# Kernel optimization log

Measured on AMD Instinct MI355X. Metric: run time of the kernel, lower is better.

## Reference

```python
import jax, jax.numpy as jnp
import numpy as np

B, S, D = 2, 2048, 1024
E, N, HID = 8, 4, 4096

def setup_inputs() -> dict:
    key = jax.random.key(0)
    ks = jax.random.split(key, 6)
    x = jax.random.normal(ks[0], (B, S, D), dtype=jnp.float32)
    w_router = jax.random.normal(ks[1], (E, D), dtype=jnp.float32) * 0.02
    A_fc = jax.random.normal(ks[2], (E, N, N, N), dtype=jnp.float32) * 0.5
    S_fc = jax.random.normal(ks[3], (E, N, HID // N, D // N), dtype=jnp.float32) * (1.0 / np.sqrt(D))
    A_proj = jax.random.normal(ks[4], (E, N, N, N), dtype=jnp.float32) * 0.5
    S_proj = jax.random.normal(ks[5], (E, N, D // N, HID // N), dtype=jnp.float32) * (1.0 / np.sqrt(HID))
    return {"x": x, "w_router": w_router, "A_fc": A_fc, "S_fc": S_fc, "A_proj": A_proj, "S_proj": S_proj}

def _phm(Xn, A, S):
    # Xn: [T, n, s_in], S: [n, s_out, s_in], A: [n, n, n] -> [T, n, s_out]
    T_ = jnp.einsum('bkl,iol->bkio', Xn, S)
    return jnp.einsum('ijk,bkio->bjo', A, T_)

def reference(x, w_router, A_fc, S_fc, A_proj, S_proj):
    e_num, n = A_fc.shape[0], A_fc.shape[1]
    d = x.shape[-1]
    flat = x.reshape(-1, d)                      # [T, D]
    T = flat.shape[0]
    logits = flat @ w_router.T                   # [T, E]
    probs = jax.nn.softmax(logits, axis=-1)
    expert_idx = jnp.argmax(logits, axis=-1)     # [T]
    tpe = jnp.zeros((e_num,), flat.dtype).at[expert_idx].add(1.0)
    frac = tpe / T
    aux_loss = jnp.sum(frac * probs.mean(axis=0)) * e_num
    Xn = flat.reshape(T, n, d // n)
    out = jnp.zeros_like(flat)
    for e in range(e_num):                        # small fixed expert loop
        h = _phm(Xn, A_fc[e], S_fc[e]).reshape(T, -1)   # [T, HID]
        h = jnp.where(h >= 0, h, 0.5 * h)               # leaky_relu slope 0.5
        Hn = (h * h).reshape(T, n, -1)
        y = _phm(Hn, A_proj[e], S_proj[e]).reshape(T, d)
        out = out + jnp.where((expert_idx == e)[:, None], y, jnp.zeros((), flat.dtype))
    return out.reshape(x.shape), aux_loss
```

## Files before the change

### kernel.cpp

```cpp
#include <hip/hip_runtime.h>
#include <hip/hip_bf16.h>


#define T_TOK 4096
#define DIM   1024
#define NEXP  8
#define HIDD  4096
#define SLOTS 5120

static constexpr size_t OFF_WFC   = 0;
static constexpr size_t OFF_WPROJ = 67108864ull;
static constexpr size_t OFF_XB    = 134217728ull;
static constexpr size_t OFF_H     = 144703488ull;
static constexpr size_t OFF_BSUM  = 186646528ull;
static constexpr size_t OFF_EIDX  = OFF_BSUM + 1024*8*8;
static constexpr size_t OFF_TOK   = OFF_EIDX + (size_t)T_TOK*4;
static constexpr size_t OFF_CNT   = OFF_TOK + (size_t)SLOTS*4;

typedef __attribute__((ext_vector_type(8))) short short8;
typedef __attribute__((ext_vector_type(4))) float f32x4;

static __device__ __forceinline__ ushort f2bf(float f) {
    __hip_bfloat16 h = __float2bfloat16(f);
    return __builtin_bit_cast(ushort, h);
}

static __device__ __forceinline__ void gload_lds16(const ushort* g, ushort* l) {
    __builtin_amdgcn_global_load_lds((const __attribute__((address_space(1))) void*)g,
                                     (__attribute__((address_space(3))) void*)l,
                                     16, 0, 0);
}

__global__ __launch_bounds__(256) void router_k(const float* __restrict__ x,
                                                const float* __restrict__ wr,
                                                double* __restrict__ bsum,
                                                int* __restrict__ eidx,
                                                ushort* __restrict__ xb)
{
    __shared__ double shp[4][8];
    int tid = threadIdx.x, w = tid >> 6, lane = tid & 63;
    int t = blockIdx.x * 4 + w;
    const float4* xr = (const float4*)(x + (size_t)t * DIM);
    float4 xv[4];
#pragma unroll
    for (int q = 0; q < 4; q++) xv[q] = xr[q * 64 + lane];
    ushort4* xo = (ushort4*)(xb + (size_t)t * DIM);
#pragma unroll
    for (int q = 0; q < 4; q++) {
        float4 v = xv[q];
        ushort4 bq;
        bq.x = f2bf(v.x); bq.y = f2bf(v.y); bq.z = f2bf(v.z); bq.w = f2bf(v.w);
        xo[q * 64 + lane] = bq;
    }
    double lg[8];
#pragma unroll
    for (int e = 0; e < 8; e++) {
        const float4* wv = (const float4*)(wr + (size_t)e * DIM);
        double s = 0.0;
#pragma unroll
        for (int q = 0; q < 4; q++) {
            float4 a = xv[q], b = wv[q * 64 + lane];
            s += (double)a.x * b.x + (double)a.y * b.y + (double)a.z * b.z + (double)a.w * b.w;
        }
#pragma unroll
        for (int d = 1; d < 64; d <<= 1) s += __shfl_xor(s, d);
        lg[e] = s;
    }
    double m = lg[0];
#pragma unroll
    for (int e = 1; e < 8; e++) m = lg[e] > m ? lg[e] : m;
    double ex[8], sum = 0.0;
#pragma unroll
    for (int e = 0; e < 8; e++) { ex[e] = exp(lg[e] - m); sum += ex[e]; }
    if (lane < 8) shp[w][lane] = ex[lane] / sum;
    if (lane == 0) {
        int am = 0; double bv = lg[0];
#pragma unroll
        for (int e = 1; e < 8; e++) if (lg[e] > bv) { bv = lg[e]; am = e; }
        eidx[t] = am;
    }
    __syncthreads();
    if (tid < 8)
        bsum[(size_t)blockIdx.x * 8 + tid] =
            shp[0][tid] + shp[1][tid] + shp[2][tid] + shp[3][tid];
}

__global__ __launch_bounds__(256) void plan_k(const double* __restrict__ bsum,
                                              const int* __restrict__ eidx,
                                              int* __restrict__ counts,
                                              int* __restrict__ offsets,
                                              int* __restrict__ tok,
                                              float* __restrict__ auxout)
{
    __shared__ int hist[256][8];
    __shared__ double red[256][8];
    __shared__ int offs[8];
    int tid = threadIdx.x;
    for (int i = tid; i < SLOTS; i += 256) tok[i] = -1;
    int base = tid * 16;
    int le[16];
    int lc[8] = {0,0,0,0,0,0,0,0};
#pragma unroll
    for (int j = 0; j < 16; j++) { le[j] = eidx[base + j]; lc[le[j]]++; }
#pragma unroll
    for (int e = 0; e < 8; e++) hist[tid][e] = lc[e];
    __syncthreads();
    for (int s = 1; s < 256; s <<= 1) {
        int v[8];
        if (tid >= s) {
#pragma unroll
            for (int e = 0; e < 8; e++) v[e] = hist[tid - s][e];
        }
        __syncthreads();
        if (tid >= s) {
#pragma unroll
            for (int e = 0; e < 8; e++) hist[tid][e] += v[e];
        }
        __syncthreads();
    }
    int myBase[8];
#pragma unroll
    for (int e = 0; e < 8; e++) myBase[e] = hist[tid][e] - lc[e];
    if (tid == 0) {
        int off = 0;
#pragma unroll
        for (int e = 0; e < 8; e++) {
            int c = hist[255][e];
            counts[e] = c;
            offsets[e] = off; offs[e] = off;
            off += (c + 127) & ~127;
        }
    }
    __syncthreads();
    int cur[8];
#pragma unroll
    for (int e = 0; e < 8; e++) cur[e] = myBase[e];
#pragma unroll
    for (int j = 0; j < 16; j++) {
        int e = le[j];
        tok[offs[e] + cur[e]++] = base + j;
    }
    double ps[8] = {0, 0, 0, 0, 0, 0, 0, 0};
    for (int b = tid; b < 1024; b += 256) {
#pragma unroll
        for (int e = 0; e < 8; e++) ps[e] += bsum[(size_t)b * 8 + e];
    }
#pragma unroll
    for (int e = 0; e < 8; e++) red[tid][e] = ps[e];
    __syncthreads();
    for (int s = 128; s > 0; s >>= 1) {
        if (tid < s) {
#pragma unroll
            for (int e = 0; e < 8; e++) red[tid][e] += red[tid + s][e];
        }
        __syncthreads();
    }
    if (tid == 0) {
        double aux = 0.0;
#pragma unroll
        for (int e = 0; e < 8; e++)
            aux += ((double)hist[255][e] / T_TOK) * (red[0][e] / T_TOK);
        auxout[0] = (float)(aux * NEXP);
    }
}

__global__ __launch_bounds__(256) void wmat_k(const float* __restrict__ Afc,
                                              const float* __restrict__ Sfc,
                                              const float* __restrict__ Apj,
                                              const float* __restrict__ Spj,
                                              ushort* __restrict__ Wfc,
                                              ushort* __restrict__ Wpj)
{
    __shared__ float Ash[64];
    int b = blockIdx.x;
    int tid = threadIdx.x;
    if (b < 8192) {
        int e = b >> 10, o = b & 1023;
        if (tid < 64) Ash[tid] = Afc[e * 64 + tid];
        __syncthreads();
        float s0 = Sfc[((size_t)(e * 4 + 0) * 1024 + o) * 256 + tid];
        float s1 = Sfc[((size_t)(e * 4 + 1) * 1024 + o) * 256 + tid];
        float s2 = Sfc[((size_t)(e * 4 + 2) * 1024 + o) * 256 + tid];
        float s3 = Sfc[((size_t)(e * 4 + 3) * 1024 + o) * 256 + tid];
        size_t base = (size_t)e * 4194304ull;
#pragma unroll
        for (int j = 0; j < 4; j++)
#pragma unroll
            for (int k = 0; k < 4; k++) {
                float v = Ash[j * 4 + k] * s0 + Ash[16 + j * 4 + k] * s1 +
                          Ash[32 + j * 4 + k] * s2 + Ash[48 + j * 4 + k] * s3;
                Wfc[base + (size_t)(j * 1024 + o) * 1024 + k * 256 + tid] = f2bf(v);
            }
    } else {
        int b2 = b - 8192;
        int e = b2 >> 8, o = b2 & 255;
        if (tid < 64) Ash[tid] = Apj[e * 64 + tid];
        __syncthreads();
        float s[4][4];
#pragma unroll
        for (int i = 0; i < 4; i++)
#pragma unroll
            for (int q = 0; q < 4; q++)
                s[i][q] = Spj[((size_t)(e * 4 + i) * 256 + o) * 1024 + q * 256 + tid];
        size_t base = (size_t)e * 4194304ull;
#pragma unroll
        for (int j = 0; j < 4; j++)
#pragma unroll
            for (int k = 0; k < 4; k++) {
                float a0 = Ash[j * 4 + k], a1 = Ash[16 + j * 4 + k];
                float a2 = Ash[32 + j * 4 + k], a3 = Ash[48 + j * 4 + k];
#pragma unroll
                for (int q = 0; q < 4; q++) {
                    float v = a0 * s[0][q] + a1 * s[1][q] + a2 * s[2][q] + a3 * s[3][q];
                    Wpj[base + (size_t)(j * 256 + o) * 4096 + k * 1024 + q * 256 + tid] = f2bf(v);
                }
            }
    }
}

template <int KDIM, int NDIM, int BM, bool FC>
__global__ __launch_bounds__(256, 2) void moe_gemm_k(const ushort* __restrict__ Abuf,
                                                     const ushort* __restrict__ Wbuf,
                                                     ushort* __restrict__ Hout,
                                                     float* __restrict__ Yout,
                                                     const int* __restrict__ counts,
                                                     const int* __restrict__ offsets,
                                                     const int* __restrict__ tok)
{
    __shared__ __align__(16) ushort As[BM * 64];
    __shared__ __align__(16) ushort Bs[256 * 64];
    constexpr int NT = KDIM / 64;
    constexpr int NF = FC ? 8 : 4;
    constexpr int WNC = FC ? 128 : 64;
    int b = blockIdx.x;
    int nb, ms;
    if (FC) {
        int r = b >> 3;
        nb = (b & 7) * 2 + r / 40;
        ms = r % 40;
    } else {
        nb = b & 3;
        ms = b >> 2;
    }
    int e = -1, mt = 0, acct = 0;
#pragma unroll
    for (int i = 0; i < 8; i++) {
        int tiles = (counts[i] + BM - 1) / BM;
        if (e < 0 && ms < acct + tiles) { e = i; mt = ms - acct; }
        acct += tiles;
    }
    if (e < 0) return;
    int m_base = offsets[e] + mt * BM;
    int n_base = nb * 256;
    int tid = threadIdx.x, w = tid >> 6, lane = tid & 63;
    int wm = FC ? (w >> 1) : 0;
    int wn = FC ? (w & 1) : w;
    const ushort* Bb = Wbuf + (size_t)e * NDIM * KDIM + (size_t)n_base * KDIM;
    int lr = lane >> 3;
    int lcs = (((lane & 7) ^ lr) << 3);
    const ushort* arow[BM / 32];
#pragma unroll
    for (int i = 0; i < BM / 32; i++) {
        int sl = m_base + i * 32 + w * 8 + lr;
        int rt = sl;
        if (FC) { rt = tok[sl]; if (rt < 0) rt = 0; }
        arow[i] = Abuf + (size_t)rt * KDIM + lcs;
    }
    f32x4 acc[4][NF];
#pragma unroll
    for (int i = 0; i < 4; i++)
#pragma unroll
        for (int j = 0; j < NF; j++) acc[i][j] = (f32x4){0.f, 0.f, 0.f, 0.f};

    for (int t = 0; t < NT; t++) {
        int k0 = t * 64;
#pragma unroll
        for (int i = 0; i < BM / 32; i++)
            gload_lds16(arow[i] + k0, &As[(i * 32 + w * 8) * 64]);
#pragma unroll
        for (int i = 0; i < 8; i++) {
            int r0 = i * 32 + w * 8;
            gload_lds16(Bb + (size_t)(r0 + lr) * KDIM + k0 + lcs, &Bs[r0 * 64]);
        }
        __syncthreads();
#pragma unroll
        for (int ks = 0; ks < 2; ks++) {
            short8 a[4], bfr[NF];
            int ca = (((ks * 4 + (lane >> 4)) ^ (lane & 7)) << 3);
#pragma unroll
            for (int f = 0; f < 4; f++)
                a[f] = *(const short8*)&As[(wm * 64 + f * 16 + (lane & 15)) * 64 + ca];
#pragma unroll
            for (int f = 0; f < NF; f++)
                bfr[f] = *(const short8*)&Bs[(wn * WNC + f * 16 + (lane & 15)) * 64 + ca];
#pragma unroll
            for (int mf = 0; mf < 4; mf++)
#pragma unroll
                for (int nf = 0; nf < NF; nf++)
                    acc[mf][nf] = __builtin_amdgcn_mfma_f32_16x16x32_bf16(a[mf], bfr[nf], acc[mf][nf], 0, 0, 0);
        }
        __syncthreads();
    }

    int col0 = n_base + wn * WNC;
    int row0 = wm * 64 + (lane >> 4) * 4;
    if (FC) {
#pragma unroll
        for (int mf = 0; mf < 4; mf++)
#pragma unroll
            for (int nf = 0; nf < NF; nf++) {
                int col = col0 + nf * 16 + (lane & 15);
#pragma unroll
                for (int rg = 0; rg < 4; rg++) {
                    float v = acc[mf][nf][rg];
                    v = v >= 0.f ? v : 0.5f * v;
                    v = v * v;
                    Hout[(size_t)(m_base + row0 + mf * 16 + rg) * NDIM + col] = f2bf(v);
                }
            }
    } else {
        int limit = offsets[e] + counts[e];
#pragma unroll
        for (int mf = 0; mf < 4; mf++) {
            int tk[4]; bool vld[4];
#pragma unroll
            for (int rg = 0; rg < 4; rg++) {
                int slot = m_base + row0 + mf * 16 + rg;
                vld[rg] = slot < limit;
                tk[rg] = vld[rg] ? tok[slot] : 0;
            }
#pragma unroll
            for (int nf = 0; nf < NF; nf++) {
                int col = col0 + nf * 16 + (lane & 15);
#pragma unroll
                for (int rg = 0; rg < 4; rg++)
                    if (vld[rg]) Yout[(size_t)tk[rg] * NDIM + col] = acc[mf][nf][rg];
            }
        }
    }
}

extern "C" void kernel_launch(void* const* d_in, const int* in_sizes, int n_in,
                              void* d_out, int out_size, void* d_ws, size_t ws_size,
                              hipStream_t stream)
{
    const float* x    = (const float*)d_in[0];
    const float* wr   = (const float*)d_in[1];
    const float* A_fc = (const float*)d_in[2];
    const float* S_fc = (const float*)d_in[3];
    const float* A_pj = (const float*)d_in[4];
    const float* S_pj = (const float*)d_in[5];
    float* out = (float*)d_out;
    char* ws = (char*)d_ws;

    ushort* Wfc   = (ushort*)(ws + OFF_WFC);
    ushort* Wpj   = (ushort*)(ws + OFF_WPROJ);
    ushort* xb    = (ushort*)(ws + OFF_XB);
    ushort* h     = (ushort*)(ws + OFF_H);
    double* bsum  = (double*)(ws + OFF_BSUM);
    int*    eidx  = (int*)(ws + OFF_EIDX);
    int*    tok   = (int*)(ws + OFF_TOK);
    int*    counts  = (int*)(ws + OFF_CNT);
    int*    offsets = counts + 16;

    router_k<<<T_TOK / 4, 256, 0, stream>>>(x, wr, bsum, eidx, xb);
    plan_k<<<1, 256, 0, stream>>>(bsum, eidx, counts, offsets, tok,
                                  out + (size_t)T_TOK * DIM);
    wmat_k<<<10240, 256, 0, stream>>>(A_fc, S_fc, A_pj, S_pj, Wfc, Wpj);
    moe_gemm_k<1024, 4096, 128, true><<<640, 256, 0, stream>>>(xb, Wfc, h, nullptr, counts, offsets, tok);
    moe_gemm_k<4096, 1024, 64, false><<<320, 256, 0, stream>>>(h, Wpj, nullptr, out, counts, offsets, tok);
}
```

Measured before the change: 195.3 us.

## Merge weight-building into router and FC GEMM launches; split-K the projection GEMM

Result: no change. 194.0 us (-0.7%).

```diff
diff --git a/kernel.cpp b/kernel.cpp
--- a/kernel.cpp
+++ b/kernel.cpp
@@ -31,58 +31,83 @@
                                      16, 0, 0);
 }
 
-__global__ __launch_bounds__(256) void router_k(const float* __restrict__ x,
-                                                const float* __restrict__ wr,
-                                                double* __restrict__ bsum,
-                                                int* __restrict__ eidx,
-                                                ushort* __restrict__ xb)
+__global__ __launch_bounds__(256) void front_k(const float* __restrict__ x,
+                                               const float* __restrict__ wr,
+                                               double* __restrict__ bsum,
+                                               int* __restrict__ eidx,
+                                               ushort* __restrict__ xb,
+                                               const float* __restrict__ Afc,
+                                               const float* __restrict__ Sfc,
+                                               ushort* __restrict__ Wfc)
 {
     __shared__ double shp[4][8];
-    int tid = threadIdx.x, w = tid >> 6, lane = tid & 63;
-    int t = blockIdx.x * 4 + w;
-    const float4* xr = (const float4*)(x + (size_t)t * DIM);
-    float4 xv[4];
-#pragma unroll
-    for (int q = 0; q < 4; q++) xv[q] = xr[q * 64 + lane];
-    ushort4* xo = (ushort4*)(xb + (size_t)t * DIM);
-#pragma unroll
-    for (int q = 0; q < 4; q++) {
-        float4 v = xv[q];
-        ushort4 bq;
-        bq.x = f2bf(v.x); bq.y = f2bf(v.y); bq.z = f2bf(v.z); bq.w = f2bf(v.w);
-        xo[q * 64 + lane] = bq;
-    }
-    double lg[8];
-#pragma unroll
-    for (int e = 0; e < 8; e++) {
-        const float4* wv = (const float4*)(wr + (size_t)e * DIM);
-        double s = 0.0;
+    __shared__ float Ash[64];
+    int tid = threadIdx.x;
+    if (blockIdx.x < 1024) {
+        int w = tid >> 6, lane = tid & 63;
+        int t = blockIdx.x * 4 + w;
+        const float4* xr = (const float4*)(x + (size_t)t * DIM);
+        float4 xv[4];
+#pragma unroll
+        for (int q = 0; q < 4; q++) xv[q] = xr[q * 64 + lane];
+        ushort4* xo = (ushort4*)(xb + (size_t)t * DIM);
 #pragma unroll
         for (int q = 0; q < 4; q++) {
-            float4 a = xv[q], b = wv[q * 64 + lane];
-            s += (double)a.x * b.x + (double)a.y * b.y + (double)a.z * b.z + (double)a.w * b.w;
-        }
-#pragma unroll
-        for (int d = 1; d < 64; d <<= 1) s += __shfl_xor(s, d);
-        lg[e] = s;
-    }
-    double m = lg[0];
-#pragma unroll
-    for (int e = 1; e < 8; e++) m = lg[e] > m ? lg[e] : m;
-    double ex[8], sum = 0.0;
-#pragma unroll
-    for (int e = 0; e < 8; e++) { ex[e] = exp(lg[e] - m); sum += ex[e]; }
-    if (lane < 8) shp[w][lane] = ex[lane] / sum;
-    if (lane == 0) {
-        int am = 0; double bv = lg[0];
-#pragma unroll
-        for (int e = 1; e < 8; e++) if (lg[e] > bv) { bv = lg[e]; am = e; }
-        eidx[t] = am;
-    }
-    __syncthreads();
-    if (tid < 8)
-        bsum[(size_t)blockIdx.x * 8 + tid] =
-            shp[0][tid] + shp[1][tid] + shp[2][tid] + shp[3][tid];
+            float4 v = xv[q];
+            ushort4 bq;
+            bq.x = f2bf(v.x); bq.y = f2bf(v.y); bq.z = f2bf(v.z); bq.w = f2bf(v.w);
+            xo[q * 64 + lane] = bq;
+        }
+        double lg[8];
+#pragma unroll
+        for (int e = 0; e < 8; e++) {
+            const float4* wv = (const float4*)(wr + (size_t)e * DIM);
+            double s = 0.0;
+#pragma unroll
+            for (int q = 0; q < 4; q++) {
+                float4 a = xv[q], b = wv[q * 64 + lane];
+                s += (double)a.x * b.x + (double)a.y * b.y + (double)a.z * b.z + (double)a.w * b.w;
+            }
+#pragma unroll
+            for (int d = 1; d < 64; d <<= 1) s += __shfl_xor(s, d);
+            lg[e] = s;
+        }
+        double m = lg[0];
+#pragma unroll
+        for (int e = 1; e < 8; e++) m = lg[e] > m ? lg[e] : m;
+        double ex[8], sum = 0.0;
+#pragma unroll
+        for (int e = 0; e < 8; e++) { ex[e] = exp(lg[e] - m); sum += ex[e]; }
+        if (lane < 8) shp[w][lane] = ex[lane] / sum;
+        if (lane == 0) {
+            int am = 0; double bv = lg[0];
+#pragma unroll
+            for (int e = 1; e < 8; e++) if (lg[e] > bv) { bv = lg[e]; am = e; }
+            eidx[t] = am;
+        }
+        __syncthreads();
+        if (tid < 8)
+            bsum[(size_t)blockIdx.x * 8 + tid] =
+                shp[0][tid] + shp[1][tid] + shp[2][tid] + shp[3][tid];
+    } else {
+        int b2 = blockIdx.x - 1024;
+        int e = b2 >> 10, o = b2 & 1023;
+        if (tid < 64) Ash[tid] = Afc[e * 64 + tid];
+        __syncthreads();
+        float s0 = Sfc[((size_t)(e * 4 + 0) * 1024 + o) * 256 + tid];
+        float s1 = Sfc[((size_t)(e * 4 + 1) * 1024 + o) * 256 + tid];
+        float s2 = Sfc[((size_t)(e * 4 + 2) * 1024 + o) * 256 + tid];
+        float s3 = Sfc[((size_t)(e * 4 + 3) * 1024 + o) * 256 + tid];
+        size_t base = (size_t)e * 4194304ull;
+#pragma unroll
+        for (int j = 0; j < 4; j++)
+#pragma unroll
+            for (int k = 0; k < 4; k++) {
+                float v = Ash[j * 4 + k] * s0 + Ash[16 + j * 4 + k] * s1 +
+                          Ash[32 + j * 4 + k] * s2 + Ash[48 + j * 4 + k] * s3;
+                Wfc[base + (size_t)(j * 1024 + o) * 1024 + k * 256 + tid] = f2bf(v);
+            }
+    }
 }
 
 __global__ __launch_bounds__(256) void plan_k(const double* __restrict__ bsum,
@@ -164,37 +189,25 @@
     }
 }
 
-__global__ __launch_bounds__(256) void wmat_k(const float* __restrict__ Afc,
-                                              const float* __restrict__ Sfc,
-                                              const float* __restrict__ Apj,
-                                              const float* __restrict__ Spj,
-                                              ushort* __restrict__ Wfc,
-                                              ushort* __restrict__ Wpj)
+__global__ __launch_bounds__(256, 2) void mid_k(const ushort* __restrict__ xb,
+                                                const ushort* __restrict__ Wfc,
+                                                ushort* __restrict__ h,
+                                                const int* __restrict__ counts,
+                                                const int* __restrict__ offsets,
+                                                const int* __restrict__ tok,
+                                                const float* __restrict__ Apj,
+                                                const float* __restrict__ Spj,
+                                                ushort* __restrict__ Wpj)
 {
-    __shared__ float Ash[64];
+    __shared__ __align__(16) ushort As[128 * 64];
+    __shared__ __align__(16) ushort Bs[256 * 64];
+    __shared__ float Ashf[64];
     int b = blockIdx.x;
     int tid = threadIdx.x;
-    if (b < 8192) {
-        int e = b >> 10, o = b & 1023;
-        if (tid < 64) Ash[tid] = Afc[e * 64 + tid];
-        __syncthreads();
-        float s0 = Sfc[((size_t)(e * 4 + 0) * 1024 + o) * 256 + tid];
-        float s1 = Sfc[((size_t)(e * 4 + 1) * 1024 + o) * 256 + tid];
-        float s2 = Sfc[((size_t)(e * 4 + 2) * 1024 + o) * 256 + tid];
-        float s3 = Sfc[((size_t)(e * 4 + 3) * 1024 + o) * 256 + tid];
-        size_t base = (size_t)e * 4194304ull;
-#pragma unroll
-        for (int j = 0; j < 4; j++)
-#pragma unroll
-            for (int k = 0; k < 4; k++) {
-                float v = Ash[j * 4 + k] * s0 + Ash[16 + j * 4 + k] * s1 +
-                          Ash[32 + j * 4 + k] * s2 + Ash[48 + j * 4 + k] * s3;
-                Wfc[base + (size_t)(j * 1024 + o) * 1024 + k * 256 + tid] = f2bf(v);
-            }
-    } else {
-        int b2 = b - 8192;
+    if (b >= 640) {
+        int b2 = b - 640;
         int e = b2 >> 8, o = b2 & 255;
-        if (tid < 64) Ash[tid] = Apj[e * 64 + tid];
+        if (tid < 64) Ashf[tid] = Apj[e * 64 + tid];
         __syncthreads();
         float s[4][4];
 #pragma unroll
@@ -207,75 +220,53 @@
         for (int j = 0; j < 4; j++)
 #pragma unroll
             for (int k = 0; k < 4; k++) {
-                float a0 = Ash[j * 4 + k], a1 = Ash[16 + j * 4 + k];
-                float a2 = Ash[32 + j * 4 + k], a3 = Ash[48 + j * 4 + k];
+                float a0 = Ashf[j * 4 + k], a1 = Ashf[16 + j * 4 + k];
+                float a2 = Ashf[32 + j * 4 + k], a3 = Ashf[48 + j * 4 + k];
 #pragma unroll
                 for (int q = 0; q < 4; q++) {
                     float v = a0 * s[0][q] + a1 * s[1][q] + a2 * s[2][q] + a3 * s[3][q];
                     Wpj[base + (size_t)(j * 256 + o) * 4096 + k * 1024 + q * 256 + tid] = f2bf(v);
                 }
             }
-    }
-}
-
-template <int KDIM, int NDIM, int BM, bool FC>
-__global__ __launch_bounds__(256, 2) void moe_gemm_k(const ushort* __restrict__ Abuf,
-                                                     const ushort* __restrict__ Wbuf,
-                                                     ushort* __restrict__ Hout,
-                                                     float* __restrict__ Yout,
-                                                     const int* __restrict__ counts,
-                                                     const int* __restrict__ offsets,
-                                                     const int* __restrict__ tok)
-{
-    __shared__ __align__(16) ushort As[BM * 64];
-    __shared__ __align__(16) ushort Bs[256 * 64];
-    constexpr int NT = KDIM / 64;
-    constexpr int NF = FC ? 8 : 4;
-    constexpr int WNC = FC ? 128 : 64;
-    int b = blockIdx.x;
-    int nb, ms;
-    if (FC) {
-        int r = b >> 3;
-        nb = (b & 7) * 2 + r / 40;
-        ms = r % 40;
-    } else {
-        nb = b & 3;
-        ms = b >> 2;
-    }
+        return;
+    }
+    constexpr int KDIM = 1024;
+    constexpr int NDIM = 4096;
+    int r = b >> 3;
+    int nb = (b & 7) * 2 + r / 40;
+    int ms = r % 40;
     int e = -1, mt = 0, acct = 0;
 #pragma unroll
     for (int i = 0; i < 8; i++) {
-        int tiles = (counts[i] + BM - 1) / BM;
+        int tiles = (counts[i] + 127) >> 7;
         if (e < 0 && ms < acct + tiles) { e = i; mt = ms - acct; }
         acct += tiles;
     }
     if (e < 0) return;
-    int m_base = offsets[e] + mt * BM;
+    int m_base = offsets[e] + mt * 128;
     int n_base = nb * 256;
-    int tid = threadIdx.x, w = tid >> 6, lane = tid & 63;
-    int wm = FC ? (w >> 1) : 0;
-    int wn = FC ? (w & 1) : w;
-    const ushort* Bb = Wbuf + (size_t)e * NDIM * KDIM + (size_t)n_base * KDIM;
+    int w = tid >> 6, lane = tid & 63;
+    int wm = w >> 1, wn = w & 1;
+    const ushort* Bb = Wfc + (size_t)e * NDIM * KDIM + (size_t)n_base * KDIM;
     int lr = lane >> 3;
     int lcs = (((lane & 7) ^ lr) << 3);
-    const ushort* arow[BM / 32];
-#pragma unroll
-    for (int i = 0; i < BM / 32; i++) {
+    const ushort* arow[4];
+#pragma unroll
+    for (int i = 0; i < 4; i++) {
         int sl = m_base + i * 32 + w * 8 + lr;
-        int rt = sl;
-        if (FC) { rt = tok[sl]; if (rt < 0) rt = 0; }
-        arow[i] = Abuf + (size_t)rt * KDIM + lcs;
-    }
-    f32x4 acc[4][NF];
+        int rt = tok[sl]; if (rt < 0) rt = 0;
+        arow[i] = xb + (size_t)rt * KDIM + lcs;
+    }
+    f32x4 acc[4][8];
 #pragma unroll
     for (int i = 0; i < 4; i++)
 #pragma unroll
-        for (int j = 0; j < NF; j++) acc[i][j] = (f32x4){0.f, 0.f, 0.f, 0.f};
-
-    for (int t = 0; t < NT; t++) {
+        for (int j = 0; j < 8; j++) acc[i][j] = (f32x4){0.f, 0.f, 0.f, 0.f};
+
+    for (int t = 0; t < KDIM / 64; t++) {
         int k0 = t * 64;
 #pragma unroll
-        for (int i = 0; i < BM / 32; i++)
+        for (int i = 0; i < 4; i++)
             gload_lds16(arow[i] + k0, &As[(i * 32 + w * 8) * 64]);
 #pragma unroll
         for (int i = 0; i < 8; i++) {
@@ -285,57 +276,130 @@
         __syncthreads();
 #pragma unroll
         for (int ks = 0; ks < 2; ks++) {
-            short8 a[4], bfr[NF];
+            short8 a[4], bfr[8];
             int ca = (((ks * 4 + (lane >> 4)) ^ (lane & 7)) << 3);
 #pragma unroll
             for (int f = 0; f < 4; f++)
                 a[f] = *(const short8*)&As[(wm * 64 + f * 16 + (lane & 15)) * 64 + ca];
 #pragma unroll
-            for (int f = 0; f < NF; f++)
-                bfr[f] = *(const short8*)&Bs[(wn * WNC + f * 16 + (lane & 15)) * 64 + ca];
+            for (int f = 0; f < 8; f++)
+                bfr[f] = *(const short8*)&Bs[(wn * 128 + f * 16 + (lane & 15)) * 64 + ca];
 #pragma unroll
             for (int mf = 0; mf < 4; mf++)
 #pragma unroll
-                for (int nf = 0; nf < NF; nf++)
+                for (int nf = 0; nf < 8; nf++)
                     acc[mf][nf] = __builtin_amdgcn_mfma_f32_16x16x32_bf16(a[mf], bfr[nf], acc[mf][nf], 0, 0, 0);
         }
         __syncthreads();
     }
 
-    int col0 = n_base + wn * WNC;
+    int col0 = n_base + wn * 128;
     int row0 = wm * 64 + (lane >> 4) * 4;
-    if (FC) {
-#pragma unroll
-        for (int mf = 0; mf < 4; mf++)
-#pragma unroll
-            for (int nf = 0; nf < NF; nf++) {
-                int col = col0 + nf * 16 + (lane & 15);
-#pragma unroll
-                for (int rg = 0; rg < 4; rg++) {
-                    float v = acc[mf][nf][rg];
-                    v = v >= 0.f ? v : 0.5f * v;
-                    v = v * v;
-                    Hout[(size_t)(m_base + row0 + mf * 16 + rg) * NDIM + col] = f2bf(v);
-                }
+#pragma unroll
+    for (int mf = 0; mf < 4; mf++)
+#pragma unroll
+        for (int nf = 0; nf < 8; nf++) {
+            int col = col0 + nf * 16 + (lane & 15);
+#pragma unroll
+            for (int rg = 0; rg < 4; rg++) {
+                float v = acc[mf][nf][rg];
+                v = v >= 0.f ? v : 0.5f * v;
+                v = v * v;
+                h[(size_t)(m_base + row0 + mf * 16 + rg) * NDIM + col] = f2bf(v);
             }
-    } else {
-        int limit = offsets[e] + counts[e];
-#pragma unroll
-        for (int mf = 0; mf < 4; mf++) {
-            int tk[4]; bool vld[4];
-#pragma unroll
-            for (int rg = 0; rg < 4; rg++) {
-                int slot = m_base + row0 + mf * 16 + rg;
-                vld[rg] = slot < limit;
-                tk[rg] = vld[rg] ? tok[slot] : 0;
-            }
-#pragma unroll
-            for (int nf = 0; nf < NF; nf++) {
-                int col = col0 + nf * 16 + (lane & 15);
-#pragma unroll
-                for (int rg = 0; rg < 4; rg++)
-                    if (vld[rg]) Yout[(size_t)tk[rg] * NDIM + col] = acc[mf][nf][rg];
-            }
+        }
+}
+
+__global__ __launch_bounds__(256, 2) void proj_k(const ushort* __restrict__ h,
+                                                 const ushort* __restrict__ Wpj,
+                                                 float* __restrict__ out,
+                                                 const int* __restrict__ counts,
+                                                 const int* __restrict__ offsets,
+                                                 const int* __restrict__ tok)
+{
+    __shared__ __align__(16) ushort As[128 * 64];
+    __shared__ __align__(16) ushort Bs[256 * 64];
+    constexpr int KDIM = 4096;
+    constexpr int NDIM = 1024;
+    constexpr int KSUB = 2048;
+    int b = blockIdx.x;
+    int nb = (b & 7) >> 1;
+    int split = b & 1;
+    int ms = b >> 3;
+    int e = -1, mt = 0, acct = 0;
+#pragma unroll
+    for (int i = 0; i < 8; i++) {
+        int tiles = (counts[i] + 127) >> 7;
+        if (e < 0 && ms < acct + tiles) { e = i; mt = ms - acct; }
+        acct += tiles;
+    }
+    if (e < 0) return;
+    int m_base = offsets[e] + mt * 128;
+    int n_base = nb * 256;
+    int tid = threadIdx.x, w = tid >> 6, lane = tid & 63;
+    int wm = w >> 1, wn = w & 1;
+    int lr = lane >> 3;
+    int lcs = (((lane & 7) ^ lr) << 3);
+    int kbase = split * KSUB;
+    const ushort* Bb = Wpj + (size_t)e * NDIM * KDIM + (size_t)n_base * KDIM + kbase;
+    const ushort* arow[4];
+#pragma unroll
+    for (int i = 0; i < 4; i++)
+        arow[i] = h + (size_t)(m_base + i * 32 + w * 8 + lr) * KDIM + kbase + lcs;
+    f32x4 acc[4][8];
+#pragma unroll
+    for (int i = 0; i < 4; i++)
+#pragma unroll
+        for (int j = 0; j < 8; j++) acc[i][j] = (f32x4){0.f, 0.f, 0.f, 0.f};
+
+    for (int t = 0; t < KSUB / 64; t++) {
+        int k0 = t * 64;
+#pragma unroll
+        for (int i = 0; i < 4; i++)
+            gload_lds16(arow[i] + k0, &As[(i * 32 + w * 8) * 64]);
+#pragma unroll
+        for (int i = 0; i < 8; i++) {
+            int r0 = i * 32 + w * 8;
+            gload_lds16(Bb + (size_t)(r0 + lr) * KDIM + k0 + lcs, &Bs[r0 * 64]);
+        }
+        __syncthreads();
+#pragma unroll
+        for (int ks = 0; ks < 2; ks++) {
+            short8 a[4], bfr[8];
+            int ca = (((ks * 4 + (lane >> 4)) ^ (lane & 7)) << 3);
+#pragma unroll
+            for (int f = 0; f < 4; f++)
+                a[f] = *(const short8*)&As[(wm * 64 + f * 16 + (lane & 15)) * 64 + ca];
+#pragma unroll
+            for (int f = 0; f < 8; f++)
+                bfr[f] = *(const short8*)&Bs[(wn * 128 + f * 16 + (lane & 15)) * 64 + ca];
+#pragma unroll
+            for (int mf = 0; mf < 4; mf++)
+#pragma unroll
+                for (int nf = 0; nf < 8; nf++)
+                    acc[mf][nf] = __builtin_amdgcn_mfma_f32_16x16x32_bf16(a[mf], bfr[nf], acc[mf][nf], 0, 0, 0);
+        }
+        __syncthreads();
+    }
+
+    int col0 = n_base + wn * 128;
+    int row0 = wm * 64 + (lane >> 4) * 4;
+    int limit = offsets[e] + counts[e];
+#pragma unroll
+    for (int mf = 0; mf < 4; mf++) {
+        int tk[4]; bool vld[4];
+#pragma unroll
+        for (int rg = 0; rg < 4; rg++) {
+            int slot = m_base + row0 + mf * 16 + rg;
+            vld[rg] = slot < limit;
+            tk[rg] = vld[rg] ? tok[slot] : 0;
+        }
+#pragma unroll
+        for (int nf = 0; nf < 8; nf++) {
+            int col = col0 + nf * 16 + (lane & 15);
+#pragma unroll
+            for (int rg = 0; rg < 4; rg++)
+                if (vld[rg]) unsafeAtomicAdd(&out[(size_t)tk[rg] * NDIM + col], acc[mf][nf][rg]);
         }
     }
 }
@@ -363,10 +427,11 @@
     int*    counts  = (int*)(ws + OFF_CNT);
     int*    offsets = counts + 16;
 
-    router_k<<<T_TOK / 4, 256, 0, stream>>>(x, wr, bsum, eidx, xb);
+    hipMemsetAsync(out, 0, (size_t)T_TOK * DIM * sizeof(float), stream);
+    front_k<<<1024 + 8192, 256, 0, stream>>>(x, wr, bsum, eidx, xb, A_fc, S_fc, Wfc);
     plan_k<<<1, 256, 0, stream>>>(bsum, eidx, counts, offsets, tok,
                                   out + (size_t)T_TOK * DIM);
-    wmat_k<<<10240, 256, 0, stream>>>(A_fc, S_fc, A_pj, S_pj, Wfc, Wpj);
-    moe_gemm_k<1024, 4096, 128, true><<<640, 256, 0, stream>>>(xb, Wfc, h, nullptr, counts, offsets, tok);
-    moe_gemm_k<4096, 1024, 64, false><<<320, 256, 0, stream>>>(h, Wpj, nullptr, out, counts, offsets, tok);
-}
+    mid_k<<<640 + 2048, 256, 0, stream>>>(xb, Wfc, h, counts, offsets, tok,
+                                          A_pj, S_pj, Wpj);
+    proj_k<<<320, 256, 0, stream>>>(h, Wpj, out, counts, offsets, tok);
+}
```
